# Optimization experiments

Hardware: AMD Instinct MI355X
Metric: run time of the kernel (lower is better)

The kernel has to match this reference:

```python
import jax, jax.numpy as jnp
import numpy as np

VOC, MEM, NSLOTS, NSENT, MAXLEN, QLEN, ANSLEN, B = 32000, 128, 20, 128, 32, 16, 8, 64


def _xavier(k, shape):
    fan_out, fan_in = shape
    std = jnp.sqrt(2.0 / (fan_in + fan_out))
    return (jax.random.normal(k, shape, jnp.float32) * std).astype(jnp.float32)


def setup_inputs() -> dict:
    key = jax.random.key(0)
    ks = jax.random.split(key, 12)
    inp = {}
    inp["input_ids"] = jax.random.randint(ks[0], (B, NSENT, MAXLEN), 0, VOC)
    inp["question"] = jax.random.randint(ks[1], (B, QLEN), 0, VOC)
    inp["ans"] = jax.random.randint(ks[2], (B, ANSLEN, 2), 0, VOC)
    E = jax.random.normal(ks[3], (VOC, MEM), jnp.float32)
    inp["E"] = E.at[0].set(0.0)  # padding_idx=0
    inp["Uw"] = _xavier(ks[4], (MEM, MEM)); inp["Ub"] = jnp.zeros((MEM,), jnp.float32)
    inp["Vw"] = _xavier(ks[5], (MEM, MEM)); inp["Vb"] = jnp.zeros((MEM,), jnp.float32)
    inp["Ww"] = _xavier(ks[6], (MEM, MEM)); inp["Wb"] = jnp.zeros((MEM,), jnp.float32)
    inp["slot_keys"] = jax.random.normal(ks[7], (NSLOTS, MEM), jnp.float32)  # self.w
    inp["Hw"] = _xavier(ks[8], (MEM, MEM)); inp["Hb"] = jnp.zeros((MEM,), jnp.float32)
    return inp


def reference(input_ids, question, ans, E, Uw, Ub, Vw, Vb, Ww, Wb, slot_keys, Hw, Hb):
    E0 = E.at[0].set(0.0)  # padding row stays zero
    bsz = input_ids.shape[0]
    n_sent = input_ids.shape[1]
    tok = input_ids.reshape(bsz, -1)
    # original indexes s[:, t, :] for t < n_sent over the flattened story
    s = E0[tok[:, :n_sent]]                       # [B, T, m]
    Ws = jnp.einsum('btm,nm->btn', s, Ww) + Wb    # precompute W(s_t): [B, T, m]
    Vkey = slot_keys @ Vw.T + Vb                  # [J, m]

    def step(mem, xs):
        # mem: [B, J, m]
        s_t, ws_t = xs                            # [B, m], [B, m]
        g = jax.nn.sigmoid(jnp.einsum('bm,bjm->bj', s_t, mem) + s_t @ slot_keys.T)  # [B, J]
        h_cand = jax.nn.relu(
            jnp.einsum('bjm,nm->bjn', mem, Uw) + Ub
            + Vkey[None, :, :] + ws_t[:, None, :]
        )  # dropout is identity in eval mode
        mem = mem + g[..., None] * h_cand
        # torch.norm(mem_j): global Frobenius norm over (batch, mem) per slot
        norms = jnp.sqrt(jnp.sum(mem * mem, axis=(0, 2), keepdims=True))
        return mem / norms, None

    mem0 = jnp.zeros((bsz, slot_keys.shape[0], s.shape[-1]), s.dtype)
    h, _ = jax.lax.scan(step, mem0, (jnp.swapaxes(s, 0, 1), jnp.swapaxes(Ws, 0, 1)))
    # output module
    q = E0[question].mean(1)                      # [B, m]
    a1 = E0[ans[:, :, 0]].mean(1)                 # [B, m]
    a2 = E0[ans[:, :, 1]].mean(1)                 # [B, m]
    p = jax.nn.softmax(jnp.einsum('bjm,bm->bj', h, q), axis=-1)   # [B, J]
    u = jnp.einsum('bj,bjm->bm', p, h)            # [B, m]
    r = jax.nn.relu(q + u @ Hw.T + Hb)            # [B, m]
    y1 = jnp.sum(r * a1, axis=1)
    y2 = jnp.sum(r * a2, axis=1)
    return jax.nn.softmax(jnp.stack((y1, y2), axis=1), axis=1)
```

## Files before the change

kernel.cpp:

```cpp
#include <hip/hip_runtime.h>
#include <math.h>


typedef __attribute__((ext_vector_type(8)))  short bf16x8;
typedef __attribute__((ext_vector_type(16))) float f32x16;

__device__ __forceinline__ unsigned short f2bh(float x) {
    unsigned int u = __float_as_uint(x);
    u += 0x7FFFu + ((u >> 16) & 1u);
    return (unsigned short)(u >> 16);
}

__device__ __forceinline__ float dpp_xor1_add(float x) {
    int y = __builtin_amdgcn_update_dpp(0, __float_as_int(x), 0xB1, 0xF, 0xF, true);
    return x + __int_as_float(y);
}
__device__ __forceinline__ float dpp_xor2_add(float x) {
    int y = __builtin_amdgcn_update_dpp(0, __float_as_int(x), 0x4E, 0xF, 0xF, true);
    return x + __int_as_float(y);
}

#define LDS_BARRIER() do {                                   \
    asm volatile("s_waitcnt lgkmcnt(0)" ::: "memory");       \
    __builtin_amdgcn_s_barrier();                            \
    asm volatile("" ::: "memory");                           \
} while (0)

__global__ __launch_bounds__(128) void prep_kernel(
    const int* __restrict__ ids, const int* __restrict__ ques, const int* __restrict__ ans,
    const float* __restrict__ E, const float* __restrict__ Ww, const float* __restrict__ Wb,
    const float* __restrict__ Vw, const float* __restrict__ Vb, const float* __restrict__ skeys,
    unsigned short* __restrict__ sTb, float* __restrict__ WsT, float* __restrict__ vkey,
    float* __restrict__ qv, float* __restrict__ a1v, float* __restrict__ a2v,
    float* __restrict__ SK)
{
    const int bi  = blockIdx.x;
    const int tid = threadIdx.x;
    __shared__ float s_l[8][132];
    __shared__ float sk_l[20 * 132];
    __shared__ float k_l[128];
    if (bi < 1024) {
        const int b = bi >> 4;
        const int g = bi & 15;
        for (int r = tid; r < 2560; r += 128) sk_l[(r >> 7) * 132 + (r & 127)] = skeys[r];
        for (int tt = 0; tt < 8; ++tt) {
            const int t     = g * 8 + tt;
            const int token = ids[b * 4096 + t];
            const float v   = E[token * 128 + tid];
            s_l[tt][tid] = v;
            sTb[(t * 64 + b) * 128 + tid] = f2bh(v);
        }
        __syncthreads();
        float acc[8];
        const float wbn = Wb[tid];
        #pragma unroll
        for (int i = 0; i < 8; ++i) acc[i] = wbn;
        const float4* wrow = (const float4*)(Ww + tid * 128);
        for (int m4 = 0; m4 < 32; ++m4) {
            const float4 w = wrow[m4];
            #pragma unroll
            for (int tt = 0; tt < 8; ++tt) {
                acc[tt] += s_l[tt][m4*4+0]*w.x + s_l[tt][m4*4+1]*w.y
                         + s_l[tt][m4*4+2]*w.z + s_l[tt][m4*4+3]*w.w;
            }
        }
        for (int tt = 0; tt < 8; ++tt)
            WsT[((g*8+tt) * 64 + b) * 128 + tid] = acc[tt];
        for (int idx = tid; idx < 160; idx += 128) {
            const int tt = idx / 20;
            const int jj = idx - tt * 20;
            float d = 0.f;
            for (int m = 0; m < 128; ++m) d += s_l[tt][m] * sk_l[jj * 132 + m];
            SK[(jj * 128 + (g*8 + tt)) * 64 + b] = d;
        }
    } else if (bi < 1044) {
        const int j = bi - 1024;
        k_l[tid] = skeys[j * 128 + tid];
        __syncthreads();
        float acc = Vb[tid];
        const float4* vrow = (const float4*)(Vw + tid * 128);
        for (int m4 = 0; m4 < 32; ++m4) {
            const float4 w = vrow[m4];
            acc += k_l[m4*4]*w.x + k_l[m4*4+1]*w.y + k_l[m4*4+2]*w.z + k_l[m4*4+3]*w.w;
        }
        vkey[j * 128 + tid] = acc;
    } else {
        const int b = bi - 1044;
        float sq = 0.f, s1 = 0.f, s2 = 0.f;
        for (int i = 0; i < 16; ++i) sq += E[ques[b*16+i] * 128 + tid];
        for (int i = 0; i < 8;  ++i) s1 += E[ans[(b*8+i)*2+0] * 128 + tid];
        for (int i = 0; i < 8;  ++i) s2 += E[ans[(b*8+i)*2+1] * 128 + tid];
        qv [b*128+tid] = sq * (1.f/16.f);
        a1v[b*128+tid] = s1 * 0.125f;
        a2v[b*128+tid] = s2 * 0.125f;
    }
}

__global__ __launch_bounds__(512, 1) void scan_kernel(
    const unsigned short* __restrict__ sTb, const float* __restrict__ WsT,
    const float* __restrict__ vkey, const float* __restrict__ Uw,
    const float* __restrict__ Ub, const float* __restrict__ SK,
    float* __restrict__ h_out)
{
    __shared__ unsigned short AB[64 * 136];
    __shared__ float g_l[64];
    __shared__ float wred[8];

    const int j    = blockIdx.x;
    const int tid  = threadIdx.x;
    const int wave = tid >> 6;
    const int lane = tid & 63;
    const int l32  = lane & 31;
    const int q    = lane >> 5;
    const int bt2  = wave & 1;
    const int nt2  = wave >> 1;
    const int n    = nt2 * 32 + l32;

    const int  grow  = bt2 * 32 + l32;
    const int  rstar = ((l32 >> 3) << 2) | (l32 & 3);
    const bool act   = (((l32 >> 2) & 1) == q);

    bf16x8 b_h[8];
    {
        const int k0 = q * 8;
        #pragma unroll
        for (int kc = 0; kc < 8; ++kc) {
            const float4* src = (const float4*)(Uw + n * 128 + kc * 16 + k0);
            const float4 v0 = src[0], v1 = src[1];
            const float xs[8] = {v0.x,v0.y,v0.z,v0.w, v1.x,v1.y,v1.z,v1.w};
            #pragma unroll
            for (int e = 0; e < 8; ++e) b_h[kc][e] = (short)f2bh(xs[e]);
        }
    }
    for (int i = tid; i < 64 * 136 / 2; i += 512) ((unsigned int*)AB)[i] = 0u;
    const float ubv = Ub[n] + vkey[j * 128 + n];

    unsigned woffB[16];
    #pragma unroll
    for (int r = 0; r < 16; ++r) {
        const int brow = bt2*32 + 4*q + (r & 3) + 8*(r >> 2);
        woffB[r] = (unsigned)((brow * 128 + n) * 4);
    }
    const char* SKj  = (const char*)SK + (size_t)j * 32768;
    const char* sfb  = (const char*)sTb + (size_t)grow * 256;

    float xprev[16];
    #pragma unroll
    for (int r = 0; r < 16; ++r) xprev[r] = 0.f;

    float  wsv[16];
    bf16x8 sf[8];
    float  skg = 0.f;
    {
        const char* pW = (const char*)WsT;
        #pragma unroll
        for (int r = 0; r < 16; ++r) wsv[r] = *(const float*)(pW + woffB[r]);
        if (wave < 2) {
            #pragma unroll
            for (int kc = 0; kc < 8; ++kc)
                sf[kc] = *(const bf16x8*)(sfb + kc * 32 + q * 16);
            skg = *(const float*)(SKj + grow * 4);
        }
    }
    __syncthreads();

    float inv_s = 1.f;

    for (int t = 0; t < 128; ++t) {
        const int tn = (t < 127) ? t + 1 : 127;

        float wsvu[16];
        #pragma unroll
        for (int r = 0; r < 16; ++r) wsvu[r] = wsv[r] + ubv;

        f32x16 acc0 = {0.f,0.f,0.f,0.f,0.f,0.f,0.f,0.f,
                       0.f,0.f,0.f,0.f,0.f,0.f,0.f,0.f};
        f32x16 acc1 = acc0;
        const unsigned short* arow = AB + (bt2*32 + l32) * 136 + q * 8;
        #pragma unroll
        for (int kc = 0; kc < 8; ++kc) {
            const bf16x8 a = *(const bf16x8*)(arow + kc * 16);
            if (kc & 1) acc1 = __builtin_amdgcn_mfma_f32_32x32x16_bf16(a, b_h[kc], acc1, 0, 0, 0);
            else        acc0 = __builtin_amdgcn_mfma_f32_32x32x16_bf16(a, b_h[kc], acc0, 0, 0, 0);
        }
        acc0 += acc1;

        if (wave < 2) {
            f32x16 gc0 = {0.f,0.f,0.f,0.f,0.f,0.f,0.f,0.f,
                          0.f,0.f,0.f,0.f,0.f,0.f,0.f,0.f};
            f32x16 gc1 = gc0;
            #pragma unroll
            for (int kc = 0; kc < 8; ++kc) {
                const bf16x8 a = *(const bf16x8*)(arow + kc * 16);
                if (kc & 1) gc1 = __builtin_amdgcn_mfma_f32_32x32x16_bf16(a, sf[kc], gc1, 0, 0, 0);
                else        gc0 = __builtin_amdgcn_mfma_f32_32x32x16_bf16(a, sf[kc], gc0, 0, 0, 0);
            }
            gc0 += gc1;
            float dsum = 0.f;
            #pragma unroll
            for (int r = 0; r < 16; ++r) dsum = (r == rstar) ? gc0[r] : dsum;
            if (act) {
                const float e = __expf(-(inv_s * dsum + skg));
                g_l[grow] = __builtin_amdgcn_rcpf(1.f + e);
            }
        }
        LDS_BARRIER();

        const float4 gA = *(const float4*)(g_l + bt2*32 + 4*q + 0);
        const float4 gB = *(const float4*)(g_l + bt2*32 + 4*q + 8);
        const float4 gC = *(const float4*)(g_l + bt2*32 + 4*q + 16);
        const float4 gD = *(const float4*)(g_l + bt2*32 + 4*q + 24);
        const float gr[16] = {gA.x,gA.y,gA.z,gA.w, gB.x,gB.y,gB.z,gB.w,
                              gC.x,gC.y,gC.z,gC.w, gD.x,gD.y,gD.z,gD.w};
        float sq0 = 0.f, sq1 = 0.f;
        #pragma unroll
        for (int r = 0; r < 16; ++r) {
            const int brow = bt2*32 + 4*q + (r & 3) + 8*(r >> 2);
            float hr = fmaf(inv_s, acc0[r], wsvu[r]);
            hr = fmaxf(hr, 0.f);
            const float x = fmaf(inv_s, xprev[r], gr[r] * hr);
            xprev[r] = x;
            AB[brow*136 + n] = (unsigned short)(__float_as_uint(x) >> 16);
            if (r & 1) sq1 = fmaf(x, x, sq1); else sq0 = fmaf(x, x, sq0);
        }

        {
            const char* pW = (const char*)WsT + (size_t)tn * 32768;
            #pragma unroll
            for (int r = 0; r < 16; ++r)
                wsv[r] = *(const float*)(pW + woffB[r]);
            if (wave < 2) {
                const char* pS = sfb + (size_t)tn * 16384;
                #pragma unroll
                for (int kc = 0; kc < 8; ++kc)
                    sf[kc] = *(const bf16x8*)(pS + kc * 32 + q * 16);
                skg = *(const float*)(SKj + (size_t)tn * 256 + grow * 4);
            }
        }

        float ssq = sq0 + sq1;
        ssq = dpp_xor1_add(ssq);
        ssq = dpp_xor2_add(ssq);
        ssq += __shfl_xor(ssq, 4, 64);
        ssq += __shfl_xor(ssq, 8, 64);
        ssq += __shfl_xor(ssq, 16, 64);
        ssq += __shfl_xor(ssq, 32, 64);
        if (lane == 0) wred[wave] = ssq;
        LDS_BARRIER();
        const float4 w0 = *(const float4*)(wred);
        const float4 w1 = *(const float4*)(wred + 4);
        inv_s = __builtin_amdgcn_rsqf(w0.x+w0.y+w0.z+w0.w + w1.x+w1.y+w1.z+w1.w);
    }

    #pragma unroll
    for (int r = 0; r < 16; ++r) {
        const int brow = bt2*32 + 4*q + (r & 3) + 8*(r >> 2);
        h_out[(brow*20 + j)*128 + n] = inv_s * xprev[r];
    }
}

__global__ __launch_bounds__(128) void final_kernel(
    const float* __restrict__ h, const float* __restrict__ qv,
    const float* __restrict__ a1v, const float* __restrict__ a2v,
    const float* __restrict__ Hw, const float* __restrict__ Hb,
    float* __restrict__ out)
{
    const int b   = blockIdx.x;
    const int tid = threadIdx.x;
    __shared__ float hb[20][128];
    __shared__ float ql[128];
    __shared__ float ul[128];
    __shared__ float pl[20];
    __shared__ float lgt[20];
    __shared__ float red1[2], red2[2];

    for (int jj = 0; jj < 20; ++jj) hb[jj][tid] = h[(b*20+jj)*128 + tid];
    ql[tid] = qv[b*128 + tid];
    __syncthreads();
    if (tid < 20) {
        float d = 0.f;
        for (int m = 0; m < 128; ++m) d += hb[tid][m] * ql[m];
        lgt[tid] = d;
    }
    __syncthreads();
    if (tid == 0) {
        float mx = lgt[0];
        for (int jj = 1; jj < 20; ++jj) mx = fmaxf(mx, lgt[jj]);
        float s = 0.f;
        for (int jj = 0; jj < 20; ++jj) { const float e = expf(lgt[jj]-mx); pl[jj] = e; s += e; }
        const float is = 1.f / s;
        for (int jj = 0; jj < 20; ++jj) pl[jj] *= is;
    }
    __syncthreads();
    float u = 0.f;
    for (int jj = 0; jj < 20; ++jj) u += pl[jj] * hb[jj][tid];
    ul[tid] = u;
    __syncthreads();
    float acc = ql[tid] + Hb[tid];
    const float4* hwr = (const float4*)(Hw + tid*128);
    for (int m4 = 0; m4 < 32; ++m4) {
        const float4 w = hwr[m4];
        acc += ul[m4*4]*w.x + ul[m4*4+1]*w.y + ul[m4*4+2]*w.z + ul[m4*4+3]*w.w;
    }
    const float r  = fmaxf(acc, 0.f);
    float y1 = r * a1v[b*128+tid];
    float y2 = r * a2v[b*128+tid];
    #pragma unroll
    for (int mask = 1; mask < 64; mask <<= 1) {
        y1 += __shfl_xor(y1, mask, 64);
        y2 += __shfl_xor(y2, mask, 64);
    }
    if ((tid & 63) == 0) { red1[tid>>6] = y1; red2[tid>>6] = y2; }
    __syncthreads();
    if (tid == 0) {
        const float z1 = red1[0] + red1[1];
        const float z2 = red2[0] + red2[1];
        const float mx = fmaxf(z1, z2);
        const float e1 = expf(z1-mx), e2 = expf(z2-mx);
        const float s  = e1 + e2;
        out[b*2+0] = e1 / s;
        out[b*2+1] = e2 / s;
    }
}

extern "C" void kernel_launch(void* const* d_in, const int* in_sizes, int n_in,
                              void* d_out, int out_size, void* d_ws, size_t ws_size,
                              hipStream_t stream)
{
    const int*   ids  = (const int*)  d_in[0];
    const int*   ques = (const int*)  d_in[1];
    const int*   ans  = (const int*)  d_in[2];
    const float* E    = (const float*)d_in[3];
    const float* Uw   = (const float*)d_in[4];
    const float* Ubv  = (const float*)d_in[5];
    const float* Vw   = (const float*)d_in[6];
    const float* Vb   = (const float*)d_in[7];
    const float* Ww   = (const float*)d_in[8];
    const float* Wb   = (const float*)d_in[9];
    const float* sk   = (const float*)d_in[10];
    const float* Hw   = (const float*)d_in[11];
    const float* Hb   = (const float*)d_in[12];

    float* ws   = (float*)d_ws;
    unsigned short* sTb = (unsigned short*)ws;
    float* WsT  = ws    + 524288;
    float* vkey = WsT   + 1048576;
    float* qv   = vkey  + 2560;
    float* a1v  = qv    + 8192;
    float* a2v  = a1v   + 8192;
    float* h    = a2v   + 8192;
    float* SK   = h     + 163840;

    prep_kernel<<<1108, 128, 0, stream>>>(ids, ques, ans, E, Ww, Wb, Vw, Vb, sk,
                                          sTb, WsT, vkey, qv, a1v, a2v, SK);
    scan_kernel<<<20, 512, 0, stream>>>(sTb, WsT, vkey, Uw, Ubv, SK, h);
    final_kernel<<<64, 128, 0, stream>>>(h, qv, a1v, a2v, Hw, Hb, (float*)d_out);
}
```

Measured before the change: 311.2 us.

## Fuse gate dot-product into memory update epilogue and transpose MFMA output layout

Swaps the MFMA operands so each lane holds one batch row and 16 output columns. This lets the gate dot product s_t·mem be computed inside the update epilogue from the just-written fp32 values, as partial sums reduced through a small LDS array at the next step. That removes the second MFMA chain that waves 0-1 ran each step to compute the gate, plus the g_l broadcast. Loads and stores become vectorized (float4/uint2), and the s_t prefetch runs two steps ahead. The gate now uses unrounded fp32 memory instead of the bf16 copy, and the sigmoid is evaluated redundantly by every lane.

```diff
diff --git a/kernel.cpp b/kernel.cpp
--- a/kernel.cpp
+++ b/kernel.cpp
@@ -9,6 +9,11 @@
     unsigned int u = __float_as_uint(x);
     u += 0x7FFFu + ((u >> 16) & 1u);
     return (unsigned short)(u >> 16);
+}
+__device__ __forceinline__ float blo(unsigned int w) { return __uint_as_float(w << 16); }
+__device__ __forceinline__ float bhi(unsigned int w) { return __uint_as_float(w & 0xFFFF0000u); }
+__device__ __forceinline__ unsigned int packtr(float lo, float hi) {
+    return (__float_as_uint(lo) >> 16) | (__float_as_uint(hi) & 0xFFFF0000u);
 }
 
 __device__ __forceinline__ float dpp_xor1_add(float x) {
@@ -103,7 +108,7 @@
     float* __restrict__ h_out)
 {
     __shared__ unsigned short AB[64 * 136];
-    __shared__ float g_l[64];
+    __shared__ float gdp[64 * 4];
     __shared__ float wred[8];
 
     const int j    = blockIdx.x;
@@ -114,129 +119,125 @@
     const int q    = lane >> 5;
     const int bt2  = wave & 1;
     const int nt2  = wave >> 1;
-    const int n    = nt2 * 32 + l32;
-
-    const int  grow  = bt2 * 32 + l32;
-    const int  rstar = ((l32 >> 3) << 2) | (l32 & 3);
-    const bool act   = (((l32 >> 2) & 1) == q);
+    const int b    = bt2 * 32 + l32;
+    const int n0   = nt2 * 32 + 4 * q;
+    const int nrow = nt2 * 32 + l32;
 
     bf16x8 b_h[8];
     {
         const int k0 = q * 8;
         #pragma unroll
         for (int kc = 0; kc < 8; ++kc) {
-            const float4* src = (const float4*)(Uw + n * 128 + kc * 16 + k0);
+            const float4* src = (const float4*)(Uw + nrow * 128 + kc * 16 + k0);
             const float4 v0 = src[0], v1 = src[1];
             const float xs[8] = {v0.x,v0.y,v0.z,v0.w, v1.x,v1.y,v1.z,v1.w};
             #pragma unroll
             for (int e = 0; e < 8; ++e) b_h[kc][e] = (short)f2bh(xs[e]);
         }
     }
+
+    float ubv[16];
+    #pragma unroll
+    for (int g4 = 0; g4 < 4; ++g4) {
+        const float4 u4 = *(const float4*)(Ub + n0 + 8 * g4);
+        const float4 v4 = *(const float4*)(vkey + j * 128 + n0 + 8 * g4);
+        ubv[g4*4+0] = u4.x + v4.x;  ubv[g4*4+1] = u4.y + v4.y;
+        ubv[g4*4+2] = u4.z + v4.z;  ubv[g4*4+3] = u4.w + v4.w;
+    }
+
+    const char* SKj = (const char*)SK + (size_t)j * 32768;
+    const unsigned wbyte = (unsigned)((b * 128 + n0) * 4);
+    const unsigned sbyte = (unsigned)(b * 256 + n0 * 2);
+
     for (int i = tid; i < 64 * 136 / 2; i += 512) ((unsigned int*)AB)[i] = 0u;
-    const float ubv = Ub[n] + vkey[j * 128 + n];
-
-    unsigned woffB[16];
-    #pragma unroll
-    for (int r = 0; r < 16; ++r) {
-        const int brow = bt2*32 + 4*q + (r & 3) + 8*(r >> 2);
-        woffB[r] = (unsigned)((brow * 128 + n) * 4);
-    }
-    const char* SKj  = (const char*)SK + (size_t)j * 32768;
-    const char* sfb  = (const char*)sTb + (size_t)grow * 256;
+    if (tid < 256) gdp[tid] = 0.f;
 
     float xprev[16];
     #pragma unroll
     for (int r = 0; r < 16; ++r) xprev[r] = 0.f;
 
-    float  wsv[16];
-    bf16x8 sf[8];
-    float  skg = 0.f;
+    float4 wA, wB, wC, wD;
+    uint2  sA, sB, sC, sD;
+    float  skv;
     {
-        const char* pW = (const char*)WsT;
-        #pragma unroll
-        for (int r = 0; r < 16; ++r) wsv[r] = *(const float*)(pW + woffB[r]);
-        if (wave < 2) {
-            #pragma unroll
-            for (int kc = 0; kc < 8; ++kc)
-                sf[kc] = *(const bf16x8*)(sfb + kc * 32 + q * 16);
-            skg = *(const float*)(SKj + grow * 4);
-        }
+        const char* pW = (const char*)WsT + wbyte;
+        wA = *(const float4*)(pW);      wB = *(const float4*)(pW + 32);
+        wC = *(const float4*)(pW + 64); wD = *(const float4*)(pW + 96);
+        const char* pS = (const char*)sTb + 16384 + sbyte;
+        sA = *(const uint2*)(pS);      sB = *(const uint2*)(pS + 16);
+        sC = *(const uint2*)(pS + 32); sD = *(const uint2*)(pS + 48);
+        skv = *(const float*)(SKj + b * 4);
     }
     __syncthreads();
 
     float inv_s = 1.f;
 
     for (int t = 0; t < 128; ++t) {
-        const int tn = (t < 127) ? t + 1 : 127;
+        const int tn  = (t < 127) ? t + 1 : 127;
+        const int tn2 = (t < 126) ? t + 2 : 127;
+
+        const float4 gd4 = *(const float4*)(gdp + b * 4);
+        const float gsum = (gd4.x + gd4.y) + (gd4.z + gd4.w);
+        const float ge   = __expf(-fmaf(inv_s, gsum, skv));
+        const float g    = __builtin_amdgcn_rcpf(1.f + ge);
 
         float wsvu[16];
-        #pragma unroll
-        for (int r = 0; r < 16; ++r) wsvu[r] = wsv[r] + ubv;
+        wsvu[0]=wA.x+ubv[0];  wsvu[1]=wA.y+ubv[1];  wsvu[2]=wA.z+ubv[2];  wsvu[3]=wA.w+ubv[3];
+        wsvu[4]=wB.x+ubv[4];  wsvu[5]=wB.y+ubv[5];  wsvu[6]=wB.z+ubv[6];  wsvu[7]=wB.w+ubv[7];
+        wsvu[8]=wC.x+ubv[8];  wsvu[9]=wC.y+ubv[9];  wsvu[10]=wC.z+ubv[10]; wsvu[11]=wC.w+ubv[11];
+        wsvu[12]=wD.x+ubv[12]; wsvu[13]=wD.y+ubv[13]; wsvu[14]=wD.z+ubv[14]; wsvu[15]=wD.w+ubv[15];
 
         f32x16 acc0 = {0.f,0.f,0.f,0.f,0.f,0.f,0.f,0.f,
                        0.f,0.f,0.f,0.f,0.f,0.f,0.f,0.f};
         f32x16 acc1 = acc0;
-        const unsigned short* arow = AB + (bt2*32 + l32) * 136 + q * 8;
+        const unsigned short* arow = AB + b * 136 + q * 8;
         #pragma unroll
         for (int kc = 0; kc < 8; ++kc) {
             const bf16x8 a = *(const bf16x8*)(arow + kc * 16);
-            if (kc & 1) acc1 = __builtin_amdgcn_mfma_f32_32x32x16_bf16(a, b_h[kc], acc1, 0, 0, 0);
-            else        acc0 = __builtin_amdgcn_mfma_f32_32x32x16_bf16(a, b_h[kc], acc0, 0, 0, 0);
+            if (kc & 1) acc1 = __builtin_amdgcn_mfma_f32_32x32x16_bf16(b_h[kc], a, acc1, 0, 0, 0);
+            else        acc0 = __builtin_amdgcn_mfma_f32_32x32x16_bf16(b_h[kc], a, acc0, 0, 0, 0);
         }
         acc0 += acc1;
-
-        if (wave < 2) {
-            f32x16 gc0 = {0.f,0.f,0.f,0.f,0.f,0.f,0.f,0.f,
-                          0.f,0.f,0.f,0.f,0.f,0.f,0.f,0.f};
-            f32x16 gc1 = gc0;
-            #pragma unroll
-            for (int kc = 0; kc < 8; ++kc) {
-                const bf16x8 a = *(const bf16x8*)(arow + kc * 16);
-                if (kc & 1) gc1 = __builtin_amdgcn_mfma_f32_32x32x16_bf16(a, sf[kc], gc1, 0, 0, 0);
-                else        gc0 = __builtin_amdgcn_mfma_f32_32x32x16_bf16(a, sf[kc], gc0, 0, 0, 0);
-            }
-            gc0 += gc1;
-            float dsum = 0.f;
-            #pragma unroll
-            for (int r = 0; r < 16; ++r) dsum = (r == rstar) ? gc0[r] : dsum;
-            if (act) {
-                const float e = __expf(-(inv_s * dsum + skg));
-                g_l[grow] = __builtin_amdgcn_rcpf(1.f + e);
-            }
-        }
         LDS_BARRIER();
 
-        const float4 gA = *(const float4*)(g_l + bt2*32 + 4*q + 0);
-        const float4 gB = *(const float4*)(g_l + bt2*32 + 4*q + 8);
-        const float4 gC = *(const float4*)(g_l + bt2*32 + 4*q + 16);
-        const float4 gD = *(const float4*)(g_l + bt2*32 + 4*q + 24);
-        const float gr[16] = {gA.x,gA.y,gA.z,gA.w, gB.x,gB.y,gB.z,gB.w,
-                              gC.x,gC.y,gC.z,gC.w, gD.x,gD.y,gD.z,gD.w};
+        float xv[16];
         float sq0 = 0.f, sq1 = 0.f;
+        float gp0 = 0.f, gp1 = 0.f;
+        const float sp[16] = {
+            blo(sA.x), bhi(sA.x), blo(sA.y), bhi(sA.y),
+            blo(sB.x), bhi(sB.x), blo(sB.y), bhi(sB.y),
+            blo(sC.x), bhi(sC.x), blo(sC.y), bhi(sC.y),
+            blo(sD.x), bhi(sD.x), blo(sD.y), bhi(sD.y)};
         #pragma unroll
         for (int r = 0; r < 16; ++r) {
-            const int brow = bt2*32 + 4*q + (r & 3) + 8*(r >> 2);
             float hr = fmaf(inv_s, acc0[r], wsvu[r]);
             hr = fmaxf(hr, 0.f);
-            const float x = fmaf(inv_s, xprev[r], gr[r] * hr);
-            xprev[r] = x;
-            AB[brow*136 + n] = (unsigned short)(__float_as_uint(x) >> 16);
-            if (r & 1) sq1 = fmaf(x, x, sq1); else sq0 = fmaf(x, x, sq0);
-        }
-
+            const float x = fmaf(inv_s, xprev[r], g * hr);
+            xprev[r] = x; xv[r] = x;
+            if (r & 1) { sq1 = fmaf(x, x, sq1); gp1 = fmaf(x, sp[r], gp1); }
+            else       { sq0 = fmaf(x, x, sq0); gp0 = fmaf(x, sp[r], gp0); }
+        }
         {
-            const char* pW = (const char*)WsT + (size_t)tn * 32768;
-            #pragma unroll
-            for (int r = 0; r < 16; ++r)
-                wsv[r] = *(const float*)(pW + woffB[r]);
-            if (wave < 2) {
-                const char* pS = sfb + (size_t)tn * 16384;
-                #pragma unroll
-                for (int kc = 0; kc < 8; ++kc)
-                    sf[kc] = *(const bf16x8*)(pS + kc * 32 + q * 16);
-                skg = *(const float*)(SKj + (size_t)tn * 256 + grow * 4);
-            }
-        }
+            unsigned int* dst = (unsigned int*)(AB + b * 136 + n0);
+            *(uint2*)(dst +  0) = (uint2){packtr(xv[0],  xv[1]),  packtr(xv[2],  xv[3])};
+            *(uint2*)(dst +  4) = (uint2){packtr(xv[4],  xv[5]),  packtr(xv[6],  xv[7])};
+            *(uint2*)(dst +  8) = (uint2){packtr(xv[8],  xv[9]),  packtr(xv[10], xv[11])};
+            *(uint2*)(dst + 12) = (uint2){packtr(xv[12], xv[13]), packtr(xv[14], xv[15])};
+        }
+
+        {
+            const char* pW = (const char*)WsT + (size_t)tn * 32768 + wbyte;
+            wA = *(const float4*)(pW);      wB = *(const float4*)(pW + 32);
+            wC = *(const float4*)(pW + 64); wD = *(const float4*)(pW + 96);
+            const char* pS = (const char*)sTb + (size_t)tn2 * 16384 + sbyte;
+            sA = *(const uint2*)(pS);      sB = *(const uint2*)(pS + 16);
+            sC = *(const uint2*)(pS + 32); sD = *(const uint2*)(pS + 48);
+            skv = *(const float*)(SKj + (size_t)tn * 256 + b * 4);
+        }
+
+        float gp = gp0 + gp1;
+        gp += __shfl_xor(gp, 32, 64);
+        if (q == 0) gdp[b * 4 + nt2] = gp;
 
         float ssq = sq0 + sq1;
         ssq = dpp_xor1_add(ssq);
@@ -252,10 +253,13 @@
         inv_s = __builtin_amdgcn_rsqf(w0.x+w0.y+w0.z+w0.w + w1.x+w1.y+w1.z+w1.w);
     }
 
+    float* hb = h_out + ((size_t)b * 20 + j) * 128 + n0;
     #pragma unroll
-    for (int r = 0; r < 16; ++r) {
-        const int brow = bt2*32 + 4*q + (r & 3) + 8*(r >> 2);
-        h_out[(brow*20 + j)*128 + n] = inv_s * xprev[r];
+    for (int g4 = 0; g4 < 4; ++g4) {
+        float4 o;
+        o.x = inv_s * xprev[g4*4+0]; o.y = inv_s * xprev[g4*4+1];
+        o.z = inv_s * xprev[g4*4+2]; o.w = inv_s * xprev[g4*4+3];
+        *(float4*)(hb + 8 * g4) = o;
     }
 }
 
```

After: 394.2 us. +26.7%, slower.
